# Kernel optimization log

Hardware: AMD Instinct MI355X
Metric: run time of the kernel (lower is better)

Reference implementation:

```python
import jax, jax.numpy as jnp
import numpy as np

B, T, DM, H, R = 2, 2048, 1024, 16, 8
HD = DM // H
LORA_SCALE = 16.0 / R  # alpha / r


def setup_inputs() -> dict:
    key = jax.random.key(0)
    ks = jax.random.split(key, 8)
    return {
        "hidden_states": jax.random.normal(ks[0], (B, T, DM), jnp.float32),
        "attention_mask": jnp.zeros((B, 1, 1, T), jnp.float32),
        "Wq": jax.random.normal(ks[1], (DM, DM), jnp.float32) * 0.02,
        "bq": jnp.zeros((DM,), jnp.float32),
        "Aq": jax.random.normal(ks[2], (R, DM), jnp.float32) * 0.02,
        "Bq": jax.random.normal(ks[3], (DM, R), jnp.float32) * 0.02,
        "Wk": jax.random.normal(ks[4], (DM, DM), jnp.float32) * 0.02,
        "bk": jnp.zeros((DM,), jnp.float32),
        "Wv": jax.random.normal(ks[5], (DM, DM), jnp.float32) * 0.02,
        "bv": jnp.zeros((DM,), jnp.float32),
        "Av": jax.random.normal(ks[6], (R, DM), jnp.float32) * 0.02,
        "Bv": jax.random.normal(ks[7], (DM, R), jnp.float32) * 0.02,
    }


def _lora_linear(x, W, b, A, Bmat):
    # y = x W^T + b + scale * (x A^T) B^T   (lora_dropout = 0 in eval)
    return x @ W.T + b + LORA_SCALE * ((x @ A.T) @ Bmat.T)


def _heads(x):
    # [b, t, (h d)] -> [b, h, t, d]
    b, t, _ = x.shape
    return x.reshape(b, t, H, HD).transpose(0, 2, 1, 3)


def reference(hidden_states, attention_mask, Wq, bq, Aq, Bq, Wk, bk, Wv, bv, Av, Bv):
    q = _heads(_lora_linear(hidden_states, Wq, bq, Aq, Bq))
    k = _heads(hidden_states @ Wk.T + bk)
    v = _heads(_lora_linear(hidden_states, Wv, bv, Av, Bv))

    scores = jnp.einsum("bhtd,bhsd->bhts", q, k) * (HD ** -0.5)
    causal = jnp.triu(jnp.ones((T, T), dtype=bool), k=1)[None, None]
    scores = jnp.where(causal, jnp.float32(-jnp.inf), scores)
    scores = scores + attention_mask
    probs = jax.nn.softmax(scores, axis=-1)  # dropout p=0 (eval)
    attn = jnp.einsum("bhts,bhsd->bhtd", probs, v)
    # [b, h, t, d] -> [b, t, h*d]
    return attn.transpose(0, 2, 1, 3).reshape(B, T, DM)
```

## Files before the change

kernel.cpp:

```cpp
#include <hip/hip_runtime.h>
#include <hip/hip_bf16.h>

#define BB 2
#define TT 2048
#define DMM 1024
#define HH 16
#define HDD 64

typedef __attribute__((ext_vector_type(8))) short bf16x8;
typedef __attribute__((ext_vector_type(4))) short short4v;
typedef __attribute__((ext_vector_type(4))) float f32x4;

static __device__ __forceinline__ short f2bf(float f) {
    __hip_bfloat16 h = __float2bfloat16(f);
    return *reinterpret_cast<short*>(&h);
}

static __device__ __forceinline__ float ex2(float x) {
    return __builtin_amdgcn_exp2f(x);
}

static __device__ __forceinline__ void gl_lds16(const void* g, void* l) {
    __builtin_amdgcn_global_load_lds(
        (const __attribute__((address_space(1))) void*)g,
        (__attribute__((address_space(3))) void*)l, 16, 0, 0);
}

__global__ void cvt_hidden(const float* __restrict__ x, short* __restrict__ y) {
    int i = blockIdx.x * 256 + threadIdx.x;
    float4 v = reinterpret_cast<const float4*>(x)[i];
    short4v o;
    o[0] = f2bf(v.x); o[1] = f2bf(v.y); o[2] = f2bf(v.z); o[3] = f2bf(v.w);
    reinterpret_cast<short4v*>(y)[i] = o;
}

__global__ void prep_w(const float* __restrict__ Wq, const float* __restrict__ Aq, const float* __restrict__ Bq,
                       const float* __restrict__ Wk,
                       const float* __restrict__ Wv, const float* __restrict__ Av, const float* __restrict__ Bv,
                       short* __restrict__ Wqe, short* __restrict__ Wke, short* __restrict__ Wve) {
    const int mode = blockIdx.y;
    const float* W = (mode == 0) ? Wq : (mode == 1) ? Wk : Wv;
    const float* A = (mode == 0) ? Aq : Av;
    const float* Bm = (mode == 0) ? Bq : Bv;
    short* outp = (mode == 0) ? Wqe : (mode == 1) ? Wke : Wve;
    int idx = blockIdx.x * 256 + threadIdx.x;
    int n = idx >> 10, k = idx & 1023;
    float v = W[idx];
    if (mode != 1) {
        float s = 0.f;
#pragma unroll
        for (int r = 0; r < 8; ++r) s += Bm[n * 8 + r] * A[r * 1024 + k];
        v += 2.0f * s;
    }
    outp[idx] = f2bf(v);
}

__global__ __launch_bounds__(256, 3) void proj_gemm(
        const short* __restrict__ Xbf,
        const short* __restrict__ Wq, const short* __restrict__ Wk, const short* __restrict__ Wv,
        const float* __restrict__ bq, const float* __restrict__ bk, const float* __restrict__ bv,
        short* __restrict__ Qb, short* __restrict__ Kb, short* __restrict__ Vtb) {
    __shared__ __align__(16) char As[2][64 * 128];
    __shared__ __align__(16) char Bs[2][128 * 128];

    const int mode = blockIdx.z;
    const short* Wbf = (mode == 0) ? Wq : (mode == 1) ? Wk : Wv;
    const float* bias = (mode == 0) ? bq : (mode == 1) ? bk : bv;
    short* outp = (mode == 0) ? Qb : (mode == 1) ? Kb : Vtb;
    const float scale = (mode == 0) ? 0.18033688f : 1.0f;

    const int tid = threadIdx.x;
    const int wave = tid >> 6, lane = tid & 63;
    const int l15 = lane & 15, l4 = lane >> 4;
    const int bx = blockIdx.x, by = blockIdx.y;
    const int wx = 2 * (bx & 3) + (by & 1);
    const int wy = (bx >> 2) * 32 + (by >> 1);
    const int m0 = wy * 64, n0 = wx * 128;
    const int wm = (wave >> 1) * 32, wn = (wave & 1) * 64;

    const int lrow8 = lane >> 3;
    const int lchunk = lane & 7;
    const int srcoff = (lchunk ^ lrow8) * 8;

#define PROJ_STAGE(BUF, K0) do {                                                     \
    _Pragma("unroll")                                                                \
    for (int i = 0; i < 2; ++i)                                                      \
        gl_lds16(Xbf + (m0 + wave * 16 + i * 8 + lrow8) * 1024 + (K0) + srcoff,      \
                 As[BUF] + wave * 2048 + i * 1024);                                  \
    _Pragma("unroll")                                                                \
    for (int i = 0; i < 4; ++i)                                                      \
        gl_lds16(Wbf + (n0 + wave * 32 + i * 8 + lrow8) * 1024 + (K0) + srcoff,      \
                 Bs[BUF] + wave * 4096 + i * 1024);                                  \
} while (0)

#define PROJ_FRAGS(BUF, KK)                                                          \
    const int colb = (KK) * 64 + l4 * 16;                                            \
    bf16x8 wf[4], xf[2];                                                             \
    _Pragma("unroll")                                                                \
    for (int w = 0; w < 4; ++w) {                                                    \
        int r = wn + w * 16 + l15;                                                   \
        wf[w] = *reinterpret_cast<const bf16x8*>(Bs[BUF] + ((r * 128 + colb) ^ ((r & 7) << 4))); \
    }                                                                                \
    _Pragma("unroll")                                                                \
    for (int x = 0; x < 2; ++x) {                                                    \
        int r = wm + x * 16 + l15;                                                   \
        xf[x] = *reinterpret_cast<const bf16x8*>(As[BUF] + ((r * 128 + colb) ^ ((r & 7) << 4))); \
    }

#define PROJ_MFMA_T(BUF) do {                                                        \
    _Pragma("unroll")                                                                \
    for (int kk = 0; kk < 2; ++kk) {                                                 \
        PROJ_FRAGS(BUF, kk);                                                         \
        _Pragma("unroll")                                                            \
        for (int w = 0; w < 4; ++w)                                                  \
            _Pragma("unroll")                                                        \
            for (int x = 0; x < 2; ++x)                                              \
                acc[w][x] = __builtin_amdgcn_mfma_f32_16x16x32_bf16(wf[w], xf[x], acc[w][x], 0, 0, 0); \
    }                                                                                \
} while (0)

#define PROJ_MFMA_N(BUF) do {                                                        \
    _Pragma("unroll")                                                                \
    for (int kk = 0; kk < 2; ++kk) {                                                 \
        PROJ_FRAGS(BUF, kk);                                                         \
        _Pragma("unroll")                                                            \
        for (int x = 0; x < 2; ++x)                                                  \
            _Pragma("unroll")                                                        \
            for (int w = 0; w < 4; ++w)                                              \
                acc[x][w] = __builtin_amdgcn_mfma_f32_16x16x32_bf16(xf[x], wf[w], acc[x][w], 0, 0, 0); \
    }                                                                                \
} while (0)

    if (mode != 2) {
        f32x4 acc[4][2] = {};
        PROJ_STAGE(0, 0);
        __syncthreads();
        for (int t = 0; t < 16; t += 2) {
            PROJ_STAGE(1, (t + 1) * 64);
            PROJ_MFMA_T(0);
            __syncthreads();
            if (t + 2 < 16) PROJ_STAGE(0, (t + 2) * 64);
            PROJ_MFMA_T(1);
            __syncthreads();
        }
#pragma unroll
        for (int w = 0; w < 4; ++w) {
            int gnb = n0 + wn + w * 16 + l4 * 4;
            int hh = gnb >> 6, d = gnb & 63;
            float4 bv4 = *reinterpret_cast<const float4*>(bias + gnb);
#pragma unroll
            for (int x = 0; x < 2; ++x) {
                int gm = m0 + wm + x * 16 + l15;
                int bb = gm >> 11, t = gm & 2047;
                short4v o;
                o[0] = f2bf((acc[w][x][0] + bv4.x) * scale);
                o[1] = f2bf((acc[w][x][1] + bv4.y) * scale);
                o[2] = f2bf((acc[w][x][2] + bv4.z) * scale);
                o[3] = f2bf((acc[w][x][3] + bv4.w) * scale);
                *reinterpret_cast<short4v*>(outp + ((bb * 16 + hh) * 2048 + t) * 64 + d) = o;
            }
        }
    } else {
        f32x4 acc[2][4] = {};
        PROJ_STAGE(0, 0);
        __syncthreads();
        for (int t = 0; t < 16; t += 2) {
            PROJ_STAGE(1, (t + 1) * 64);
            PROJ_MFMA_N(0);
            __syncthreads();
            if (t + 2 < 16) PROJ_STAGE(0, (t + 2) * 64);
            PROJ_MFMA_N(1);
            __syncthreads();
        }
#pragma unroll
        for (int x = 0; x < 2; ++x) {
            int gmb = m0 + wm + x * 16 + l4 * 4;
            int bb = gmb >> 11, t = gmb & 2047;
#pragma unroll
            for (int w = 0; w < 4; ++w) {
                int gn = n0 + wn + w * 16 + l15;
                int hh = gn >> 6, d = gn & 63;
                int tx = ((gn >> 3) & 1) << 2;
                float bvs = bias[gn];
                short4v o;
                o[0] = f2bf(acc[x][w][0] + bvs);
                o[1] = f2bf(acc[x][w][1] + bvs);
                o[2] = f2bf(acc[x][w][2] + bvs);
                o[3] = f2bf(acc[x][w][3] + bvs);
                *reinterpret_cast<short4v*>(outp + ((bb * 16 + hh) * 64 + d) * 2048 + (t ^ tx)) = o;
            }
        }
    }
}


#define STAGE(BUF, T) do {                                                           \
    const int _kv = (T) << 5;                                                        \
    gl_lds16(Kp + (_kv + krow) * 64 + kswz, MEM + (BUF) * 4096 + wv * 1024);         \
    gl_lds16(Vp + lane * 2048 + _kv + wv * 8, MEM + 16384 + (BUF) * 4096 + wv * 1024);\
} while (0)

#define SLICEJOB(QF0, QF1, OO, M, L, QBASE) do {                                     \
    f32x4 ss = {};                                                                   \
    ss = __builtin_amdgcn_mfma_f32_16x16x32_bf16(kf0, QF0, ss, 0, 0, 0);             \
    ss = __builtin_amdgcn_mfma_f32_16x16x32_bf16(kf1, QF1, ss, 0, 0, 0);             \
    float pr[4];                                                                     \
    if (kvs + 15 > (QBASE)) {                                                        \
        _Pragma("unroll")                                                            \
        for (int r = 0; r < 4; ++r) {                                                \
            float v = ss[r] + mv[r];                                                 \
            if (kvs + l4*4 + r > (QBASE) + l15) v = -1e30f;                          \
            pr[r] = v;                                                               \
        }                                                                            \
    } else {                                                                         \
        _Pragma("unroll")                                                            \
        for (int r = 0; r < 4; ++r) pr[r] = ss[r] + mv[r];                           \
    }                                                                                \
    float tl = fmaxf(fmaxf(pr[0], pr[1]), fmaxf(pr[2], pr[3]));                      \
    if (!__all(tl - (M) <= 11.5415603f)) {                                           \
        float tm = tl;                                                               \
        tm = fmaxf(tm, __shfl_xor(tm, 16));                                          \
        tm = fmaxf(tm, __shfl_xor(tm, 32));                                          \
        float mn = fmaxf((M), tm);                                                   \
        float al = ex2((M) - mn);                                                    \
        M = mn; L *= al;                                                             \
        _Pragma("unroll")                                                            \
        for (int dt = 0; dt < 4; ++dt)                                               \
            _Pragma("unroll")                                                        \
            for (int r = 0; r < 4; ++r) OO[dt][r] *= al;                             \
    }                                                                                \
    _Pragma("unroll")                                                                \
    for (int r = 0; r < 4; ++r) pr[r] = ex2(pr[r] - (M));                            \
    L += (pr[0] + pr[1]) + (pr[2] + pr[3]);                                          \
    short4v pa;                                                                      \
    _Pragma("unroll")                                                                \
    for (int r = 0; r < 4; ++r) pa[r] = f2bf(pr[r]);                                 \
    _Pragma("unroll")                                                                \
    for (int dt = 0; dt < 4; ++dt)                                                   \
        OO[dt] = __builtin_amdgcn_mfma_f32_16x16x16bf16_1k(vf[dt], pa, OO[dt], 0, 0, 0); \
} while (0)

#define AITER(BUF, T) do {                                                           \
    if ((T) + 2 < NT) {                                                              \
        STAGE((((BUF) + 2) & 3), (T) + 2);                                           \
        asm volatile("s_waitcnt vmcnt(4)" ::: "memory");                             \
    } else if ((T) + 1 < NT) {                                                       \
        asm volatile("s_waitcnt vmcnt(2)" ::: "memory");                             \
    } else {                                                                         \
        asm volatile("s_waitcnt vmcnt(0)" ::: "memory");                             \
    }                                                                                \
    asm volatile("s_barrier" ::: "memory");                                          \
    if ((T) < nkA) {                                                                 \
        const char* Kcur = MEM + (BUF) * 4096;                                       \
        const char* Vcur = MEM + 16384 + (BUF) * 4096;                               \
        bf16x8 kf0 = *reinterpret_cast<const bf16x8*>(Kcur + kb0);                   \
        bf16x8 kf1 = *reinterpret_cast<const bf16x8*>(Kcur + (kb0 ^ 64));            \
        short4v vf[4];                                                               \
        _Pragma("unroll")                                                            \
        for (int dt = 0; dt < 4; ++dt)                                               \
            vf[dt] = *reinterpret_cast<const short4v*>(Vcur + vb0 + dt * 256);       \
        const int kvs = ((T) << 5) + 16 * s;                                         \
        float4 mv = *reinterpret_cast<const float4*>(mlds + kvs + l4 * 4);           \
        SLICEJOB(qfA0, qfA1, OA, MA, LA, qbaseA);                                    \
        if ((T) < nkB) SLICEJOB(qfB0, qfB1, OB, MB, LB, qbaseB);                     \
    }                                                                                \
} while (0)

__global__ __launch_bounds__(256, 4) void attn(
        const short* __restrict__ Qb, const short* __restrict__ Kb,
        const short* __restrict__ Vt, const float* __restrict__ amask,
        float* __restrict__ outp) {
    __shared__ __align__(16) char MEM[40960];

    const int tid = threadIdx.x, wv = tid >> 6, lane = tid & 63;
    const int l15 = lane & 15, l4 = lane >> 4;
    const int xcd = blockIdx.x & 7;
    const int k   = blockIdx.x >> 3;
    const int j   = ((k >> 5) << 3) | ((k & 3) << 1) | ((k >> 4) & 1);
    const int bh  = xcd * 4 + ((k >> 2) & 3);
    const int p  = wv & 1;
    const int s  = wv >> 1;
    const int i  = 2 * j + p;
    const int b = bh >> 4, h = bh & 15;

    const short* Qp = Qb + bh * TT * HDD;
    const short* Kp = Kb + bh * TT * HDD;
    const short* Vp = Vt + bh * HDD * TT;
    const float* mp = amask + b * TT;
    float* mlds = (float*)(MEM + 32768);

    const int qbaseA = (127 - i) << 4;
    const int qbaseB = i << 4;
    const int nkA = ((qbaseA + 15 - 16 * s) >> 5) + 1;
    const int nkB = ((qbaseB + 15 - 16 * s) >> 5) + 1;
    const int NT = ((127 - 2 * j) * 16 + 47) >> 5;

    const int krow = wv * 8 + (lane >> 3);
    const int kswz = ((lane & 7) ^ (lane >> 3)) * 8;

    const int kb0 = (16 * s + l15) * 128 + ((l4 ^ (l15 & 7)) << 4);
    const int vb0 = (2 * s + (l4 >> 1)) * 1024 + l15 * 16 + (((l4 & 1) ^ (l15 >> 3)) << 3);

    {
        int mi8 = tid * 8;
        float4 a = *reinterpret_cast<const float4*>(mp + mi8);
        float4 c = *reinterpret_cast<const float4*>(mp + mi8 + 4);
        a.x *= 1.44269504f; a.y *= 1.44269504f; a.z *= 1.44269504f; a.w *= 1.44269504f;
        c.x *= 1.44269504f; c.y *= 1.44269504f; c.z *= 1.44269504f; c.w *= 1.44269504f;
        *reinterpret_cast<float4*>(mlds + mi8) = a;
        *reinterpret_cast<float4*>(mlds + mi8 + 4) = c;
    }

    bf16x8 qfA0 = *reinterpret_cast<const bf16x8*>(Qp + (qbaseA + l15) * 64 + l4 * 8);
    bf16x8 qfA1 = *reinterpret_cast<const bf16x8*>(Qp + (qbaseA + l15) * 64 + 32 + l4 * 8);
    bf16x8 qfB0 = *reinterpret_cast<const bf16x8*>(Qp + (qbaseB + l15) * 64 + l4 * 8);
    bf16x8 qfB1 = *reinterpret_cast<const bf16x8*>(Qp + (qbaseB + l15) * 64 + 32 + l4 * 8);

    f32x4 OA[4] = {}, OB[4] = {};
    float MA = -1e30f, LA = 0.f, MB = -1e30f, LB = 0.f;

    STAGE(0, 0);
    STAGE(1, 1);
    asm volatile("s_waitcnt lgkmcnt(0)" ::: "memory");

    int t = 0;
    for (; t + 4 <= NT; t += 4) {
        AITER(0, t);
        AITER(1, t + 1);
        AITER(2, t + 2);
        AITER(3, t + 3);
    }
    for (; t < NT; ++t) AITER((t & 3), t);

    asm volatile("s_barrier" ::: "memory");

    LA += __shfl_xor(LA, 16); LA += __shfl_xor(LA, 32);
    LB += __shfl_xor(LB, 16); LB += __shfl_xor(LB, 32);

    float* mg = (float*)MEM + p * 2560 + lane * 40;
    if (s) {
#pragma unroll
        for (int dt = 0; dt < 4; ++dt) *reinterpret_cast<f32x4*>(mg + dt * 4) = OA[dt];
        mg[16] = MA; mg[17] = LA;
#pragma unroll
        for (int dt = 0; dt < 4; ++dt) *reinterpret_cast<f32x4*>(mg + 20 + dt * 4) = OB[dt];
        mg[36] = MB; mg[37] = LB;
    }
    __syncthreads();
    if (!s) {
        {
            float m1 = mg[16], l1 = mg[17];
            float ms = fmaxf(MA, m1);
            float e0 = ex2(MA - ms), e1 = ex2(m1 - ms);
            float inv = 1.0f / (LA * e0 + l1 * e1);
            int tA = qbaseA + l15;
#pragma unroll
            for (int dt = 0; dt < 4; ++dt) {
                f32x4 o1 = *reinterpret_cast<const f32x4*>(mg + dt * 4);
                float4 o;
                o.x = (OA[dt][0] * e0 + o1[0] * e1) * inv;
                o.y = (OA[dt][1] * e0 + o1[1] * e1) * inv;
                o.z = (OA[dt][2] * e0 + o1[2] * e1) * inv;
                o.w = (OA[dt][3] * e0 + o1[3] * e1) * inv;
                *reinterpret_cast<float4*>(outp + (b * 2048 + tA) * 1024 + h * 64 + dt * 16 + l4 * 4) = o;
            }
        }
        {
            float m1 = mg[36], l1 = mg[37];
            float ms = fmaxf(MB, m1);
            float e0 = ex2(MB - ms), e1 = ex2(m1 - ms);
            float inv = 1.0f / (LB * e0 + l1 * e1);
            int tB = qbaseB + l15;
#pragma unroll
            for (int dt = 0; dt < 4; ++dt) {
                f32x4 o1 = *reinterpret_cast<const f32x4*>(mg + 20 + dt * 4);
                float4 o;
                o.x = (OB[dt][0] * e0 + o1[0] * e1) * inv;
                o.y = (OB[dt][1] * e0 + o1[1] * e1) * inv;
                o.z = (OB[dt][2] * e0 + o1[2] * e1) * inv;
                o.w = (OB[dt][3] * e0 + o1[3] * e1) * inv;
                *reinterpret_cast<float4*>(outp + (b * 2048 + tB) * 1024 + h * 64 + dt * 16 + l4 * 4) = o;
            }
        }
    }
}

extern "C" void kernel_launch(void* const* d_in, const int* in_sizes, int n_in,
                              void* d_out, int out_size, void* d_ws, size_t ws_size,
                              hipStream_t stream) {
    const float* hidden = (const float*)d_in[0];
    const float* amask  = (const float*)d_in[1];
    const float* Wq = (const float*)d_in[2];
    const float* bq = (const float*)d_in[3];
    const float* Aq = (const float*)d_in[4];
    const float* Bq = (const float*)d_in[5];
    const float* Wk = (const float*)d_in[6];
    const float* bk = (const float*)d_in[7];
    const float* Wv = (const float*)d_in[8];
    const float* bv = (const float*)d_in[9];
    const float* Av = (const float*)d_in[10];
    const float* Bv = (const float*)d_in[11];
    float* outp = (float*)d_out;

    char* ws = (char*)d_ws;
    short* Xbf = (short*)(ws);
    short* Wqe = (short*)(ws + (8 << 20));
    short* Wke = (short*)(ws + (10 << 20));
    short* Wve = (short*)(ws + (12 << 20));
    short* Qb  = (short*)(ws + (14 << 20));
    short* Kb  = (short*)(ws + (22 << 20));
    short* Vtb = (short*)(ws + (30 << 20));

    cvt_hidden<<<4096, 256, 0, stream>>>(hidden, Xbf);
    prep_w<<<dim3(4096, 3), 256, 0, stream>>>(Wq, Aq, Bq, Wk, Wv, Av, Bv, Wqe, Wke, Wve);
    proj_gemm<<<dim3(8, 64, 3), 256, 0, stream>>>(Xbf, Wqe, Wke, Wve, bq, bk, bv, Qb, Kb, Vtb);
    attn<<<1024, 256, 0, stream>>>(Qb, Kb, Vtb, amask, outp);
}
```

Before: 104.2 us.

## Deepen projection GEMM pipeline to four-stage LDS ring with vmcnt waits

The projection GEMM moves from a double-buffered K=64 tile to a four-slot ring of K=32 tiles, keeping two tiles in flight. Instead of __syncthreads it uses explicit s_waitcnt vmcnt counts plus s_barrier, so global-to-LDS loads overlap the MFMA work with less stalling. The LDS swizzle is changed to suit the 64-byte row layout. Barriers become more frequent and there is less MFMA work per stage, and the hand-written wait counts rely on the exact number of outstanding loads.

Result: slower. 108.5 us (+4.1%).

```diff
diff --git a/kernel.cpp b/kernel.cpp
--- a/kernel.cpp
+++ b/kernel.cpp
@@ -60,8 +60,8 @@
         const short* __restrict__ Wq, const short* __restrict__ Wk, const short* __restrict__ Wv,
         const float* __restrict__ bq, const float* __restrict__ bk, const float* __restrict__ bv,
         short* __restrict__ Qb, short* __restrict__ Kb, short* __restrict__ Vtb) {
-    __shared__ __align__(16) char As[2][64 * 128];
-    __shared__ __align__(16) char Bs[2][128 * 128];
+    __shared__ __align__(16) char PA[4][4096];
+    __shared__ __align__(16) char PB[4][8192];
 
     const int mode = blockIdx.z;
     const short* Wbf = (mode == 0) ? Wq : (mode == 1) ? Wk : Wv;
@@ -78,39 +78,42 @@
     const int m0 = wy * 64, n0 = wx * 128;
     const int wm = (wave >> 1) * 32, wn = (wave & 1) * 64;
 
-    const int lrow8 = lane >> 3;
-    const int lchunk = lane & 7;
-    const int srcoff = (lchunk ^ lrow8) * 8;
-
-#define PROJ_STAGE(BUF, K0) do {                                                     \
-    _Pragma("unroll")                                                                \
-    for (int i = 0; i < 2; ++i)                                                      \
-        gl_lds16(Xbf + (m0 + wave * 16 + i * 8 + lrow8) * 1024 + (K0) + srcoff,      \
-                 As[BUF] + wave * 2048 + i * 1024);                                  \
-    _Pragma("unroll")                                                                \
-    for (int i = 0; i < 4; ++i)                                                      \
-        gl_lds16(Wbf + (n0 + wave * 32 + i * 8 + lrow8) * 1024 + (K0) + srcoff,      \
-                 Bs[BUF] + wave * 4096 + i * 1024);                                  \
-} while (0)
-
-#define PROJ_FRAGS(BUF, KK)                                                          \
-    const int colb = (KK) * 64 + l4 * 16;                                            \
+    const int arow = wave * 16 + (lane >> 2);
+    const int brow = wave * 32 + (lane >> 2);
+    const int srcc = ((lane & 3) ^ ((lane >> 3) & 3)) * 8;
+
+#define PSTG(BUF, T) do {                                                            \
+    const int _k0 = (T) * 32;                                                        \
+    gl_lds16(Xbf + (m0 + arow) * 1024 + _k0 + srcc, PA[BUF] + wave * 1024);          \
+    gl_lds16(Wbf + (n0 + brow) * 1024 + _k0 + srcc, PB[BUF] + wave * 2048);          \
+    gl_lds16(Wbf + (n0 + brow + 16) * 1024 + _k0 + srcc, PB[BUF] + wave * 2048 + 1024); \
+} while (0)
+
+#define PFRAG(BUF)                                                                   \
     bf16x8 wf[4], xf[2];                                                             \
     _Pragma("unroll")                                                                \
     for (int w = 0; w < 4; ++w) {                                                    \
         int r = wn + w * 16 + l15;                                                   \
-        wf[w] = *reinterpret_cast<const bf16x8*>(Bs[BUF] + ((r * 128 + colb) ^ ((r & 7) << 4))); \
+        wf[w] = *reinterpret_cast<const bf16x8*>(PB[BUF] + r * 64 + ((l4 ^ ((r >> 1) & 3)) << 4)); \
     }                                                                                \
     _Pragma("unroll")                                                                \
     for (int x = 0; x < 2; ++x) {                                                    \
         int r = wm + x * 16 + l15;                                                   \
-        xf[x] = *reinterpret_cast<const bf16x8*>(As[BUF] + ((r * 128 + colb) ^ ((r & 7) << 4))); \
-    }
-
-#define PROJ_MFMA_T(BUF) do {                                                        \
-    _Pragma("unroll")                                                                \
-    for (int kk = 0; kk < 2; ++kk) {                                                 \
-        PROJ_FRAGS(BUF, kk);                                                         \
+        xf[x] = *reinterpret_cast<const bf16x8*>(PA[BUF] + r * 64 + ((l4 ^ ((r >> 1) & 3)) << 4)); \
+    }
+
+#define PITER_T(BUF, T) do {                                                         \
+    if ((T) + 2 < 32) {                                                              \
+        PSTG((((BUF) + 2) & 3), (T) + 2);                                            \
+        asm volatile("s_waitcnt vmcnt(6)" ::: "memory");                             \
+    } else if ((T) + 1 < 32) {                                                       \
+        asm volatile("s_waitcnt vmcnt(3)" ::: "memory");                             \
+    } else {                                                                         \
+        asm volatile("s_waitcnt vmcnt(0)" ::: "memory");                             \
+    }                                                                                \
+    asm volatile("s_barrier" ::: "memory");                                          \
+    {                                                                                \
+        PFRAG(BUF);                                                                  \
         _Pragma("unroll")                                                            \
         for (int w = 0; w < 4; ++w)                                                  \
             _Pragma("unroll")                                                        \
@@ -119,10 +122,18 @@
     }                                                                                \
 } while (0)
 
-#define PROJ_MFMA_N(BUF) do {                                                        \
-    _Pragma("unroll")                                                                \
-    for (int kk = 0; kk < 2; ++kk) {                                                 \
-        PROJ_FRAGS(BUF, kk);                                                         \
+#define PITER_N(BUF, T) do {                                                         \
+    if ((T) + 2 < 32) {                                                              \
+        PSTG((((BUF) + 2) & 3), (T) + 2);                                            \
+        asm volatile("s_waitcnt vmcnt(6)" ::: "memory");                             \
+    } else if ((T) + 1 < 32) {                                                       \
+        asm volatile("s_waitcnt vmcnt(3)" ::: "memory");                             \
+    } else {                                                                         \
+        asm volatile("s_waitcnt vmcnt(0)" ::: "memory");                             \
+    }                                                                                \
+    asm volatile("s_barrier" ::: "memory");                                          \
+    {                                                                                \
+        PFRAG(BUF);                                                                  \
         _Pragma("unroll")                                                            \
         for (int x = 0; x < 2; ++x)                                                  \
             _Pragma("unroll")                                                        \
@@ -133,15 +144,13 @@
 
     if (mode != 2) {
         f32x4 acc[4][2] = {};
-        PROJ_STAGE(0, 0);
-        __syncthreads();
-        for (int t = 0; t < 16; t += 2) {
-            PROJ_STAGE(1, (t + 1) * 64);
-            PROJ_MFMA_T(0);
-            __syncthreads();
-            if (t + 2 < 16) PROJ_STAGE(0, (t + 2) * 64);
-            PROJ_MFMA_T(1);
-            __syncthreads();
+        PSTG(0, 0);
+        PSTG(1, 1);
+        for (int t = 0; t < 32; t += 4) {
+            PITER_T(0, t);
+            PITER_T(1, t + 1);
+            PITER_T(2, t + 2);
+            PITER_T(3, t + 3);
         }
 #pragma unroll
         for (int w = 0; w < 4; ++w) {
@@ -162,15 +171,13 @@
         }
     } else {
         f32x4 acc[2][4] = {};
-        PROJ_STAGE(0, 0);
-        __syncthreads();
-        for (int t = 0; t < 16; t += 2) {
-            PROJ_STAGE(1, (t + 1) * 64);
-            PROJ_MFMA_N(0);
-            __syncthreads();
-            if (t + 2 < 16) PROJ_STAGE(0, (t + 2) * 64);
-            PROJ_MFMA_N(1);
-            __syncthreads();
+        PSTG(0, 0);
+        PSTG(1, 1);
+        for (int t = 0; t < 32; t += 4) {
+            PITER_N(0, t);
+            PITER_N(1, t + 1);
+            PITER_N(2, t + 2);
+            PITER_N(3, t + 3);
         }
 #pragma unroll
         for (int x = 0; x < 2; ++x) {
```

## Fuse Q/K/V projections into one kernel sharing the X tile

Applied to the files above, without the earlier changes.

Replaces the three-way blockIdx.z projection GEMM with a single kernel where each block computes Q, K and V tiles for the same rows and columns, loading the X tile once per K-step and reusing it across three weight tiles. The K-step shrinks from 64 to 32 and the double-buffered prefetch is dropped in favour of a single buffer with two barriers per step. This is meant to cut redundant X loads and launch/tail overhead. The cost is more accumulator registers, lower occupancy, only 512 blocks, and no overlap between loads and MFMA work.

Result: no change. 102.9 us (median of 2 runs) (-1.3%).

```diff
diff --git a/kernel.cpp b/kernel.cpp
--- a/kernel.cpp
+++ b/kernel.cpp
@@ -55,19 +55,13 @@
     outp[idx] = f2bf(v);
 }
 
-__global__ __launch_bounds__(256, 3) void proj_gemm(
+__global__ __launch_bounds__(256) void proj_fused(
         const short* __restrict__ Xbf,
-        const short* __restrict__ Wq, const short* __restrict__ Wk, const short* __restrict__ Wv,
+        const short* __restrict__ Wqe, const short* __restrict__ Wke, const short* __restrict__ Wve,
         const float* __restrict__ bq, const float* __restrict__ bk, const float* __restrict__ bv,
         short* __restrict__ Qb, short* __restrict__ Kb, short* __restrict__ Vtb) {
-    __shared__ __align__(16) char As[2][64 * 128];
-    __shared__ __align__(16) char Bs[2][128 * 128];
-
-    const int mode = blockIdx.z;
-    const short* Wbf = (mode == 0) ? Wq : (mode == 1) ? Wk : Wv;
-    const float* bias = (mode == 0) ? bq : (mode == 1) ? bk : bv;
-    short* outp = (mode == 0) ? Qb : (mode == 1) ? Kb : Vtb;
-    const float scale = (mode == 0) ? 0.18033688f : 1.0f;
+    __shared__ __align__(16) char XS[4096];
+    __shared__ __align__(16) char WS[3][8192];
 
     const int tid = threadIdx.x;
     const int wave = tid >> 6, lane = tid & 63;
@@ -78,117 +72,120 @@
     const int m0 = wy * 64, n0 = wx * 128;
     const int wm = (wave >> 1) * 32, wn = (wave & 1) * 64;
 
-    const int lrow8 = lane >> 3;
-    const int lchunk = lane & 7;
-    const int srcoff = (lchunk ^ lrow8) * 8;
-
-#define PROJ_STAGE(BUF, K0) do {                                                     \
-    _Pragma("unroll")                                                                \
-    for (int i = 0; i < 2; ++i)                                                      \
-        gl_lds16(Xbf + (m0 + wave * 16 + i * 8 + lrow8) * 1024 + (K0) + srcoff,      \
-                 As[BUF] + wave * 2048 + i * 1024);                                  \
-    _Pragma("unroll")                                                                \
-    for (int i = 0; i < 4; ++i)                                                      \
-        gl_lds16(Wbf + (n0 + wave * 32 + i * 8 + lrow8) * 1024 + (K0) + srcoff,      \
-                 Bs[BUF] + wave * 4096 + i * 1024);                                  \
-} while (0)
-
-#define PROJ_FRAGS(BUF, KK)                                                          \
-    const int colb = (KK) * 64 + l4 * 16;                                            \
-    bf16x8 wf[4], xf[2];                                                             \
-    _Pragma("unroll")                                                                \
-    for (int w = 0; w < 4; ++w) {                                                    \
-        int r = wn + w * 16 + l15;                                                   \
-        wf[w] = *reinterpret_cast<const bf16x8*>(Bs[BUF] + ((r * 128 + colb) ^ ((r & 7) << 4))); \
-    }                                                                                \
-    _Pragma("unroll")                                                                \
-    for (int x = 0; x < 2; ++x) {                                                    \
-        int r = wm + x * 16 + l15;                                                   \
-        xf[x] = *reinterpret_cast<const bf16x8*>(As[BUF] + ((r * 128 + colb) ^ ((r & 7) << 4))); \
-    }
-
-#define PROJ_MFMA_T(BUF) do {                                                        \
-    _Pragma("unroll")                                                                \
-    for (int kk = 0; kk < 2; ++kk) {                                                 \
-        PROJ_FRAGS(BUF, kk);                                                         \
-        _Pragma("unroll")                                                            \
-        for (int w = 0; w < 4; ++w)                                                  \
-            _Pragma("unroll")                                                        \
-            for (int x = 0; x < 2; ++x)                                              \
-                acc[w][x] = __builtin_amdgcn_mfma_f32_16x16x32_bf16(wf[w], xf[x], acc[w][x], 0, 0, 0); \
-    }                                                                                \
-} while (0)
-
-#define PROJ_MFMA_N(BUF) do {                                                        \
-    _Pragma("unroll")                                                                \
-    for (int kk = 0; kk < 2; ++kk) {                                                 \
-        PROJ_FRAGS(BUF, kk);                                                         \
-        _Pragma("unroll")                                                            \
-        for (int x = 0; x < 2; ++x)                                                  \
-            _Pragma("unroll")                                                        \
-            for (int w = 0; w < 4; ++w)                                              \
-                acc[x][w] = __builtin_amdgcn_mfma_f32_16x16x32_bf16(xf[x], wf[w], acc[x][w], 0, 0, 0); \
-    }                                                                                \
-} while (0)
-
-    if (mode != 2) {
-        f32x4 acc[4][2] = {};
-        PROJ_STAGE(0, 0);
+    const int srow_x = wave * 16 + (lane >> 2);
+    const int srow_w = wave * 32 + (lane >> 2);
+    const int srcc = ((lane & 3) ^ ((lane >> 3) & 3)) * 8;
+
+    f32x4 aq[4][2] = {}, ak[4][2] = {}, av[2][4] = {};
+
+    for (int k0 = 0; k0 < 1024; k0 += 32) {
         __syncthreads();
-        for (int t = 0; t < 16; t += 2) {
-            PROJ_STAGE(1, (t + 1) * 64);
-            PROJ_MFMA_T(0);
-            __syncthreads();
-            if (t + 2 < 16) PROJ_STAGE(0, (t + 2) * 64);
-            PROJ_MFMA_T(1);
-            __syncthreads();
-        }
+        gl_lds16(Xbf + (m0 + srow_x) * 1024 + k0 + srcc, XS + wave * 1024);
+        gl_lds16(Wqe + (n0 + srow_w) * 1024 + k0 + srcc, WS[0] + wave * 2048);
+        gl_lds16(Wqe + (n0 + srow_w + 16) * 1024 + k0 + srcc, WS[0] + wave * 2048 + 1024);
+        gl_lds16(Wke + (n0 + srow_w) * 1024 + k0 + srcc, WS[1] + wave * 2048);
+        gl_lds16(Wke + (n0 + srow_w + 16) * 1024 + k0 + srcc, WS[1] + wave * 2048 + 1024);
+        gl_lds16(Wve + (n0 + srow_w) * 1024 + k0 + srcc, WS[2] + wave * 2048);
+        gl_lds16(Wve + (n0 + srow_w + 16) * 1024 + k0 + srcc, WS[2] + wave * 2048 + 1024);
+        __syncthreads();
+
+        bf16x8 xf[2];
+#pragma unroll
+        for (int x = 0; x < 2; ++x) {
+            int r = wm + x * 16 + l15;
+            xf[x] = *reinterpret_cast<const bf16x8*>(XS + r * 64 + ((l4 ^ ((r >> 1) & 3)) << 4));
+        }
+        {
+            bf16x8 wf[4];
+#pragma unroll
+            for (int w = 0; w < 4; ++w) {
+                int r = wn + w * 16 + l15;
+                wf[w] = *reinterpret_cast<const bf16x8*>(WS[0] + r * 64 + ((l4 ^ ((r >> 1) & 3)) << 4));
+            }
+#pragma unroll
+            for (int w = 0; w < 4; ++w)
+#pragma unroll
+                for (int x = 0; x < 2; ++x)
+                    aq[w][x] = __builtin_amdgcn_mfma_f32_16x16x32_bf16(wf[w], xf[x], aq[w][x], 0, 0, 0);
+        }
+        {
+            bf16x8 wf[4];
+#pragma unroll
+            for (int w = 0; w < 4; ++w) {
+                int r = wn + w * 16 + l15;
+                wf[w] = *reinterpret_cast<const bf16x8*>(WS[1] + r * 64 + ((l4 ^ ((r >> 1) & 3)) << 4));
+            }
+#pragma unroll
+            for (int w = 0; w < 4; ++w)
+#pragma unroll
+                for (int x = 0; x < 2; ++x)
+                    ak[w][x] = __builtin_amdgcn_mfma_f32_16x16x32_bf16(wf[w], xf[x], ak[w][x], 0, 0, 0);
+        }
+        {
+            bf16x8 wf[4];
+#pragma unroll
+            for (int w = 0; w < 4; ++w) {
+                int r = wn + w * 16 + l15;
+                wf[w] = *reinterpret_cast<const bf16x8*>(WS[2] + r * 64 + ((l4 ^ ((r >> 1) & 3)) << 4));
+            }
+#pragma unroll
+            for (int x = 0; x < 2; ++x)
+#pragma unroll
+                for (int w = 0; w < 4; ++w)
+                    av[x][w] = __builtin_amdgcn_mfma_f32_16x16x32_bf16(xf[x], wf[w], av[x][w], 0, 0, 0);
+        }
+    }
+
+#pragma unroll
+    for (int w = 0; w < 4; ++w) {
+        int gnb = n0 + wn + w * 16 + l4 * 4;
+        int hh = gnb >> 6, d = gnb & 63;
+        float4 bv4 = *reinterpret_cast<const float4*>(bq + gnb);
+#pragma unroll
+        for (int x = 0; x < 2; ++x) {
+            int gm = m0 + wm + x * 16 + l15;
+            int bb = gm >> 11, t = gm & 2047;
+            short4v o;
+            o[0] = f2bf((aq[w][x][0] + bv4.x) * 0.18033688f);
+            o[1] = f2bf((aq[w][x][1] + bv4.y) * 0.18033688f);
+            o[2] = f2bf((aq[w][x][2] + bv4.z) * 0.18033688f);
+            o[3] = f2bf((aq[w][x][3] + bv4.w) * 0.18033688f);
+            *reinterpret_cast<short4v*>(Qb + ((bb * 16 + hh) * 2048 + t) * 64 + d) = o;
+        }
+    }
+#pragma unroll
+    for (int w = 0; w < 4; ++w) {
+        int gnb = n0 + wn + w * 16 + l4 * 4;
+        int hh = gnb >> 6, d = gnb & 63;
+        float4 bv4 = *reinterpret_cast<const float4*>(bk + gnb);
+#pragma unroll
+        for (int x = 0; x < 2; ++x) {
+            int gm = m0 + wm + x * 16 + l15;
+            int bb = gm >> 11, t = gm & 2047;
+            short4v o;
+            o[0] = f2bf(ak[w][x][0] + bv4.x);
+            o[1] = f2bf(ak[w][x][1] + bv4.y);
+            o[2] = f2bf(ak[w][x][2] + bv4.z);
+            o[3] = f2bf(ak[w][x][3] + bv4.w);
+            *reinterpret_cast<short4v*>(Kb + ((bb * 16 + hh) * 2048 + t) * 64 + d) = o;
+        }
+    }
+#pragma unroll
+    for (int x = 0; x < 2; ++x) {
+        int gmb = m0 + wm + x * 16 + l4 * 4;
+        int bb = gmb >> 11, t = gmb & 2047;
 #pragma unroll
         for (int w = 0; w < 4; ++w) {
-            int gnb = n0 + wn + w * 16 + l4 * 4;
-            int hh = gnb >> 6, d = gnb & 63;
-            float4 bv4 = *reinterpret_cast<const float4*>(bias + gnb);
-#pragma unroll
-            for (int x = 0; x < 2; ++x) {
-                int gm = m0 + wm + x * 16 + l15;
-                int bb = gm >> 11, t = gm & 2047;
-                short4v o;
-                o[0] = f2bf((acc[w][x][0] + bv4.x) * scale);
-                o[1] = f2bf((acc[w][x][1] + bv4.y) * scale);
-                o[2] = f2bf((acc[w][x][2] + bv4.z) * scale);
-                o[3] = f2bf((acc[w][x][3] + bv4.w) * scale);
-                *reinterpret_cast<short4v*>(outp + ((bb * 16 + hh) * 2048 + t) * 64 + d) = o;
-            }
-        }
-    } else {
-        f32x4 acc[2][4] = {};
-        PROJ_STAGE(0, 0);
-        __syncthreads();
-        for (int t = 0; t < 16; t += 2) {
-            PROJ_STAGE(1, (t + 1) * 64);
-            PROJ_MFMA_N(0);
-            __syncthreads();
-            if (t + 2 < 16) PROJ_STAGE(0, (t + 2) * 64);
-            PROJ_MFMA_N(1);
-            __syncthreads();
-        }
-#pragma unroll
-        for (int x = 0; x < 2; ++x) {
-            int gmb = m0 + wm + x * 16 + l4 * 4;
-            int bb = gmb >> 11, t = gmb & 2047;
-#pragma unroll
-            for (int w = 0; w < 4; ++w) {
-                int gn = n0 + wn + w * 16 + l15;
-                int hh = gn >> 6, d = gn & 63;
-                int tx = ((gn >> 3) & 1) << 2;
-                float bvs = bias[gn];
-                short4v o;
-                o[0] = f2bf(acc[x][w][0] + bvs);
-                o[1] = f2bf(acc[x][w][1] + bvs);
-                o[2] = f2bf(acc[x][w][2] + bvs);
-                o[3] = f2bf(acc[x][w][3] + bvs);
-                *reinterpret_cast<short4v*>(outp + ((bb * 16 + hh) * 64 + d) * 2048 + (t ^ tx)) = o;
-            }
+            int gn = n0 + wn + w * 16 + l15;
+            int hh = gn >> 6, d = gn & 63;
+            int tx = ((gn >> 3) & 1) << 2;
+            float bvs = bv[gn];
+            short4v o;
+            o[0] = f2bf(av[x][w][0] + bvs);
+            o[1] = f2bf(av[x][w][1] + bvs);
+            o[2] = f2bf(av[x][w][2] + bvs);
+            o[3] = f2bf(av[x][w][3] + bvs);
+            *reinterpret_cast<short4v*>(Vtb + ((bb * 16 + hh) * 64 + d) * 2048 + (t ^ tx)) = o;
         }
     }
 }
@@ -413,6 +410,6 @@
 
     cvt_hidden<<<4096, 256, 0, stream>>>(hidden, Xbf);
     prep_w<<<dim3(4096, 3), 256, 0, stream>>>(Wq, Aq, Bq, Wk, Wv, Av, Bv, Wqe, Wke, Wve);
-    proj_gemm<<<dim3(8, 64, 3), 256, 0, stream>>>(Xbf, Wqe, Wke, Wve, bq, bk, bv, Qb, Kb, Vtb);
+    proj_fused<<<dim3(8, 64), 256, 0, stream>>>(Xbf, Wqe, Wke, Wve, bq, bk, bv, Qb, Kb, Vtb);
     attn<<<1024, 256, 0, stream>>>(Qb, Kb, Vtb, amask, outp);
 }
```
